# Kernel tuning notes

Hardware: AMD Instinct MI355X
Metric: run time of the kernel (lower is better)

Reference implementation:

```python
import jax, jax.numpy as jnp
import numpy as np

N_NODES = 100000
N_EDGES = 1200000
N_GRAPHS = 500
IN_DIM, HID, OUT = 128, 64, 16


def setup_inputs() -> dict:
    key = jax.random.key(0)
    ks = jax.random.split(key, 10)
    x = jax.random.normal(ks[0], (N_NODES, IN_DIM), dtype=jnp.float32)
    edge_index = jax.random.randint(ks[1], (2, N_EDGES), 0, N_NODES, dtype=jnp.int64)
    batch = jnp.sort(jax.random.randint(ks[2], (N_NODES,), 0, N_GRAPHS, dtype=jnp.int64))
    # Glorot-style init for GCN linear weights, zero bias (PyG default)
    def glorot(k, fan_in, fan_out):
        s = jnp.sqrt(6.0 / (fan_in + fan_out))
        return jax.random.uniform(k, (fan_in, fan_out), jnp.float32, -s, s)
    W1 = glorot(ks[3], IN_DIM, HID); b1 = jnp.zeros((HID,), jnp.float32)
    W2 = glorot(ks[4], HID, HID);    b2 = jnp.zeros((HID,), jnp.float32)
    W3 = glorot(ks[5], HID, OUT);    b3 = jnp.zeros((OUT,), jnp.float32)
    return {"x": x, "edge_index": edge_index, "batch": batch,
            "W1": W1, "b1": b1, "W2": W2, "b2": b2, "W3": W3, "b3": b3}


def gcn_conv(x, src, dst, deg_inv_sqrt, W, b, n_nodes):
    # PyG GCNConv: h = x @ W; aggregate with sym-normalized A+I; add bias.
    h = x @ W  # [N, F_out]
    norm = deg_inv_sqrt[src] * deg_inv_sqrt[dst]            # [E]
    msg = h[src] * norm[:, None]                            # gather + scale
    agg = jax.ops.segment_sum(msg, dst, num_segments=n_nodes)
    agg = agg + h * (deg_inv_sqrt * deg_inv_sqrt)[:, None]  # self-loop term
    return agg + b


def reference(x, edge_index, batch, W1, b1, W2, b2, W3, b3):
    n = x.shape[0]
    src, dst = edge_index[0], edge_index[1]
    # degree of A + I (count incoming edges at dst, plus self-loop)
    deg = 1.0 + jax.ops.segment_sum(jnp.ones_like(src, dtype=x.dtype), dst, num_segments=n)
    dis = deg ** -0.5  # deg >= 1 so always finite
    h = gcn_conv(x, src, dst, dis, W1, b1, n)
    h = jax.nn.relu(h)
    h = gcn_conv(h, src, dst, dis, W2, b2, n)
    h = jax.nn.relu(h)
    h = gcn_conv(h, src, dst, dis, W3, b3, n)
    # global_mean_pool over graph ids
    sums = jax.ops.segment_sum(h, batch, num_segments=N_GRAPHS)
    counts = jax.ops.segment_sum(jnp.ones((n,), h.dtype), batch, num_segments=N_GRAPHS)
    return sums / jnp.clip(counts, 1.0)[:, None]
```

## Files before the change

### kernel.cpp

```cpp
#include <hip/hip_runtime.h>
#include <hip/hip_bf16.h>
#include <hip/hip_fp16.h>

#define IN_DIM 128
#define HID    64
#define OUTF   16
#define NGRAPH 500

#define CE    2048
#define NRNG  8
#define CAP   512
#define NG    32
#define RSZ   12544

__device__ __forceinline__ uint2 f4_to_h4(float4 a) {
    __half2 lo = __floats2half2_rn(a.x, a.y);
    __half2 hi = __floats2half2_rn(a.z, a.w);
    uint2 r;
    r.x = *(unsigned*)&lo;
    r.y = *(unsigned*)&hi;
    return r;
}
__device__ __forceinline__ float4 h4_to_f4(uint2 q) {
    __half2 a = *(__half2*)&q.x, b = *(__half2*)&q.y;
    float2 fa = __half22float2(a), fb = __half22float2(b);
    return make_float4(fa.x, fa.y, fb.x, fb.y);
}
__device__ __forceinline__ void h8_to_f8(uint4 p, float4& f0, float4& f1) {
    __half2 a = *(__half2*)&p.x, b = *(__half2*)&p.y;
    __half2 c = *(__half2*)&p.z, d = *(__half2*)&p.w;
    float2 fa = __half22float2(a), fb = __half22float2(b);
    float2 fc = __half22float2(c), fd = __half22float2(d);
    f0 = make_float4(fa.x, fa.y, fb.x, fb.y);
    f1 = make_float4(fc.x, fc.y, fd.x, fd.y);
}

template<int K>
__global__ __launch_bounds__(256, 4) void gemm64_kernel(const float* __restrict__ X,
                                                        const float* __restrict__ W,
                                                        __half* __restrict__ Hh, int N) {
    constexpr int BK = 64;
    constexpr int PAD = 4;
    constexpr int LDX = BK + PAD;
    constexpr int K4 = K / 4;
    __shared__ float sX[64 * LDX];
    __shared__ float sW[BK * 64];
    const int tid = threadIdx.x;
    const int row0 = blockIdx.x * 64;
    const int tc = tid & 15;
    const int tr = tid >> 4;

    const float4* W4 = (const float4*)W;
    const float4* X4 = (const float4*)X;
    float4* sW4 = (float4*)sW;

    float4 acc0 = {0,0,0,0}, acc1 = {0,0,0,0}, acc2 = {0,0,0,0}, acc3 = {0,0,0,0};

    for (int k0 = 0; k0 < K; k0 += BK) {
        for (int i = tid; i < BK * 16; i += 256) sW4[i] = W4[k0 * 16 + i];
        for (int i = tid; i < 64 * (BK / 4); i += 256) {
            int r = i >> 4, kk = i & 15;
            int gr = row0 + r;
            float4 v = {0.f, 0.f, 0.f, 0.f};
            if (gr < N) v = X4[(long long)gr * K4 + (k0 >> 2) + kk];
            *(float4*)&sX[r * LDX + kk * 4] = v;
        }
        __syncthreads();

        const float* sX0 = &sX[(tr * 4) * LDX];
#pragma unroll 4
        for (int k = 0; k < BK; k += 4) {
            float4 x0 = *(const float4*)&sX0[k];
            float4 x1 = *(const float4*)&sX0[LDX + k];
            float4 x2 = *(const float4*)&sX0[2 * LDX + k];
            float4 x3 = *(const float4*)&sX0[3 * LDX + k];
            float4 w0 = sW4[(k + 0) * 16 + tc];
            float4 w1 = sW4[(k + 1) * 16 + tc];
            float4 w2 = sW4[(k + 2) * 16 + tc];
            float4 w3 = sW4[(k + 3) * 16 + tc];
            acc0.x += x0.x * w0.x; acc0.y += x0.x * w0.y; acc0.z += x0.x * w0.z; acc0.w += x0.x * w0.w;
            acc1.x += x1.x * w0.x; acc1.y += x1.x * w0.y; acc1.z += x1.x * w0.z; acc1.w += x1.x * w0.w;
            acc2.x += x2.x * w0.x; acc2.y += x2.x * w0.y; acc2.z += x2.x * w0.z; acc2.w += x2.x * w0.w;
            acc3.x += x3.x * w0.x; acc3.y += x3.x * w0.y; acc3.z += x3.x * w0.z; acc3.w += x3.x * w0.w;
            acc0.x += x0.y * w1.x; acc0.y += x0.y * w1.y; acc0.z += x0.y * w1.z; acc0.w += x0.y * w1.w;
            acc1.x += x1.y * w1.x; acc1.y += x1.y * w1.y; acc1.z += x1.y * w1.z; acc1.w += x1.y * w1.w;
            acc2.x += x2.y * w1.x; acc2.y += x2.y * w1.y; acc2.z += x2.y * w1.z; acc2.w += x2.y * w1.w;
            acc3.x += x3.y * w1.x; acc3.y += x3.y * w1.y; acc3.z += x3.y * w1.z; acc3.w += x3.y * w1.w;
            acc0.x += x0.z * w2.x; acc0.y += x0.z * w2.y; acc0.z += x0.z * w2.z; acc0.w += x0.z * w2.w;
            acc1.x += x1.z * w2.x; acc1.y += x1.z * w2.y; acc1.z += x1.z * w2.z; acc1.w += x1.z * w2.w;
            acc2.x += x2.z * w2.x; acc2.y += x2.z * w2.y; acc2.z += x2.z * w2.z; acc2.w += x2.z * w2.w;
            acc3.x += x3.z * w2.x; acc3.y += x3.z * w2.y; acc3.z += x3.z * w2.z; acc3.w += x3.z * w2.w;
            acc0.x += x0.w * w3.x; acc0.y += x0.w * w3.y; acc0.z += x0.w * w3.z; acc0.w += x0.w * w3.w;
            acc1.x += x1.w * w3.x; acc1.y += x1.w * w3.y; acc1.z += x1.w * w3.z; acc1.w += x1.w * w3.w;
            acc2.x += x2.w * w3.x; acc2.y += x2.w * w3.y; acc2.z += x2.w * w3.z; acc2.w += x2.w * w3.w;
            acc3.x += x3.w * w3.x; acc3.y += x3.w * w3.y; acc3.z += x3.w * w3.z; acc3.w += x3.w * w3.w;
        }
        __syncthreads();
    }

    uint2* Hh2 = (uint2*)Hh;
    int r0 = row0 + tr * 4;
    if (r0 + 0 < N) Hh2[(long long)(r0 + 0) * 16 + tc] = f4_to_h4(acc0);
    if (r0 + 1 < N) Hh2[(long long)(r0 + 1) * 16 + tc] = f4_to_h4(acc1);
    if (r0 + 2 < N) Hh2[(long long)(r0 + 2) * 16 + tc] = f4_to_h4(acc2);
    if (r0 + 3 < N) Hh2[(long long)(r0 + 3) * 16 + tc] = f4_to_h4(acc3);
}

template<int K, int F>
__global__ __launch_bounds__(256) void gemm_kernel(const float* __restrict__ X,
                                                   const float* __restrict__ W,
                                                   __half* __restrict__ Hh, int N) {
    constexpr int C4 = F / 4;
    constexpr int ROWS = 256 / C4;
    constexpr int K4 = K / 4;
    constexpr int LDX4 = K4 + 1;
    __shared__ float4 sW[K * C4];
    __shared__ float4 sX4[ROWS * LDX4];
    const int tid = threadIdx.x;
    const float4* W4 = (const float4*)W;
    for (int i = tid; i < K * C4; i += 256) sW[i] = W4[i];
    const int row0 = blockIdx.x * ROWS;
    const float4* X4 = (const float4*)X;
    for (int i = tid; i < ROWS * K4; i += 256) {
        int r = i / K4, kk = i - r * K4;
        int gr = row0 + r;
        float4 z = {0.f, 0.f, 0.f, 0.f};
        sX4[r * LDX4 + kk] = (gr < N) ? X4[(long long)gr * K4 + kk] : z;
    }
    __syncthreads();
    const int r = tid / C4, c4 = tid - (tid / C4) * C4;
    const float* sXr = (const float*)&sX4[r * LDX4];
    float4 acc = {0.f, 0.f, 0.f, 0.f};
#pragma unroll
    for (int k = 0; k < K; ++k) {
        float xv = sXr[k];
        float4 wv = sW[k * C4 + c4];
        acc.x += xv * wv.x; acc.y += xv * wv.y;
        acc.z += xv * wv.z; acc.w += xv * wv.w;
    }
    const int gr = row0 + r;
    if (gr < N) ((uint2*)Hh)[(long long)gr * C4 + c4] = f4_to_h4(acc);
}

__global__ __launch_bounds__(256) void part_kernel(const int* __restrict__ src,
                                                   const int* __restrict__ dst,
                                                   uint2* __restrict__ seg,
                                                   int* __restrict__ segcnt,
                                                   int E, int rangeSize) {
    __shared__ uint2 sSeg[NRNG][CAP];
    __shared__ int sCnt[NRNG];
    const int tid = threadIdx.x;
    if (tid < NRNG) sCnt[tid] = 0;
    __syncthreads();
    const int base = blockIdx.x * CE + tid;
    int d[8], s[8];
#pragma unroll
    for (int k = 0; k < 8; ++k) {
        int e = base + k * 256;
        d[k] = (e < E) ? dst[e] : -1;
        s[k] = (e < E) ? src[e] : 0;
    }
#pragma unroll
    for (int k = 0; k < 8; ++k) {
        if (d[k] >= 0) {
            int r = d[k] / rangeSize;
            int li = atomicAdd(&sCnt[r], 1);
            if (li < CAP) sSeg[r][li] = make_uint2((unsigned)s[k], (unsigned)d[k]);
        }
    }
    __syncthreads();
    for (int r = 0; r < NRNG; ++r) {
        int n = sCnt[r] < CAP ? sCnt[r] : CAP;
        uint2* out = seg + ((size_t)(blockIdx.x * NRNG + r)) * CAP;
        for (int i = tid; i < n; i += 256) out[i] = sSeg[r][i];
        if (tid == 0) segcnt[blockIdx.x * NRNG + r] = n;
    }
}

__global__ __launch_bounds__(256) void count_kernel(const uint2* __restrict__ seg,
                                                    const int* __restrict__ segcnt,
                                                    int* __restrict__ cnt,
                                                    int N, int rangeSize, int nchunks) {
    __shared__ int hist[RSZ];
    const int r = blockIdx.x & (NRNG - 1);
    const int g = blockIdx.x >> 3;
    const int cpg = (nchunks + NG - 1) / NG;
    const int c0 = g * cpg;
    const int c1 = (c0 + cpg < nchunks) ? c0 + cpg : nchunks;
    for (int i = threadIdx.x; i < rangeSize; i += 256) hist[i] = 0;
    __syncthreads();
    const int base = r * rangeSize;
    for (int c = c0; c < c1; ++c) {
        const int si = c * NRNG + r;
        const int n = segcnt[si];
        const uint2* s = seg + (size_t)si * CAP;
        for (int i = threadIdx.x; i < n; i += 256)
            atomicAdd(&hist[(int)s[i].y - base], 1);
    }
    __syncthreads();
    const int lim = (base + rangeSize <= N) ? rangeSize : (N - base);
    for (int i = threadIdx.x; i < lim; i += 256)
        cnt[(size_t)g * N + base + i] = hist[i];
}

__global__ __launch_bounds__(256) void nodescan_kernel(int* __restrict__ cnt,
                                                       int* __restrict__ degi, int N) {
    const int q = blockIdx.x * 256 + threadIdx.x;
    const int n0 = q * 4;
    if (n0 >= N) return;
    if ((N & 3) == 0 && n0 + 3 < N) {
        int4* c4 = (int4*)cnt;
        const int N4 = N >> 2;
        int4 run = {0, 0, 0, 0};
#pragma unroll
        for (int g = 0; g < NG; ++g) {
            const size_t idx = (size_t)g * N4 + q;
            int4 c = c4[idx];
            c4[idx] = run;
            run.x += c.x; run.y += c.y; run.z += c.z; run.w += c.w;
        }
        ((int4*)degi)[q] = run;
    } else {
        const int nend = (n0 + 4 < N) ? n0 + 4 : N;
        for (int n = n0; n < nend; ++n) {
            int run = 0;
            for (int g = 0; g < NG; ++g) {
                const size_t idx = (size_t)g * N + n;
                int c = cnt[idx];
                cnt[idx] = run;
                run += c;
            }
            degi[n] = run;
        }
    }
}

__global__ __launch_bounds__(1024) void scan1_kernel(const int* __restrict__ degi,
                                                     int* __restrict__ rowptr,
                                                     int* __restrict__ aux,
                                                     float* __restrict__ dis,
                                                     float* __restrict__ pool0, int N) {
    if (blockIdx.x == 0) {
        for (int i = threadIdx.x; i < NGRAPH * OUTF + NGRAPH; i += 1024) pool0[i] = 0.f;
    }
    __shared__ int s[1024];
    int i = blockIdx.x * 1024 + threadIdx.x;
    int v = (i < N) ? degi[i] : 0;
    if (i < N) dis[i] = rsqrtf(1.0f + (float)v);
    s[threadIdx.x] = v;
    __syncthreads();
    for (int off = 1; off < 1024; off <<= 1) {
        int t = (threadIdx.x >= off) ? s[threadIdx.x - off] : 0;
        __syncthreads();
        s[threadIdx.x] += t;
        __syncthreads();
    }
    if (i < N) rowptr[i] = s[threadIdx.x] - v;
    if (threadIdx.x == 1023) aux[blockIdx.x] = s[1023];
}

__global__ __launch_bounds__(1024) void scan3_kernel(int* __restrict__ rowptr,
                                                     const int* __restrict__ aux,
                                                     int N, int nb) {
    __shared__ int s[128];
    const int t = threadIdx.x;
    if (t < 128) s[t] = (t < nb) ? aux[t] : 0;
    __syncthreads();
    for (int off = 1; off < 128; off <<= 1) {
        int v = (t >= off && t < 128) ? s[t - off] : 0;
        __syncthreads();
        if (t < 128) s[t] += v;
        __syncthreads();
    }
    int add = (blockIdx.x == 0) ? 0 : s[blockIdx.x - 1];
    int i = blockIdx.x * 1024 + t;
    if (i < N) rowptr[i] += add;
}

__global__ __launch_bounds__(256) void scatter_kernel(const uint2* __restrict__ seg,
                                                      const int* __restrict__ segcnt,
                                                      const int* __restrict__ cntp,
                                                      const int* __restrict__ rowptr,
                                                      int* __restrict__ csr_src,
                                                      int N, int rangeSize, int nchunks) {
    __shared__ int hist[RSZ];
    const int r = blockIdx.x & (NRNG - 1);
    const int g = blockIdx.x >> 3;
    const int cpg = (nchunks + NG - 1) / NG;
    const int c0 = g * cpg;
    const int c1 = (c0 + cpg < nchunks) ? c0 + cpg : nchunks;
    for (int i = threadIdx.x; i < rangeSize; i += 256) hist[i] = 0;
    __syncthreads();
    const int base = r * rangeSize;
    for (int c = c0; c < c1; ++c) {
        const int si = c * NRNG + r;
        const int n = segcnt[si];
        const uint2* s = seg + (size_t)si * CAP;
        for (int i = threadIdx.x; i < n; i += 256) {
            uint2 v = s[i];
            const int d = (int)v.y;
            const int rank = atomicAdd(&hist[d - base], 1);
            csr_src[rowptr[d] + cntp[(size_t)g * N + d] + rank] = (int)v.x;
        }
    }
}

template<bool RELU>
__global__ __launch_bounds__(256) void agg64_kernel(const __half* __restrict__ Hh,
                                                    const int* __restrict__ rowptr,
                                                    const int* __restrict__ csr_src,
                                                    const float* __restrict__ dis,
                                                    const float4* __restrict__ b4,
                                                    float4* __restrict__ out4, int N, int E) {
    const int tid = threadIdx.x;
    const int lane = tid & 63;
    const int node = blockIdx.x * 16 + (tid >> 6) * 4 + (lane >> 4);
    const int g2 = (lane >> 3) & 1;
    const int c = lane & 7;
    if (node >= N) return;
    const uint4* Hh4 = (const uint4*)Hh;
    float dd = dis[node];
    int i0 = rowptr[node];
    int i1 = (node + 1 < N) ? rowptr[node + 1] : E;
    float4 a0 = {0.f, 0.f, 0.f, 0.f}, a1 = {0.f, 0.f, 0.f, 0.f};
    int i = i0 + g2;
    int iB = i + 2;
    int sA = (i < i1) ? csr_src[i] : 0;
    int sB = (iB < i1) ? csr_src[iB] : 0;
    uint4 pA = make_uint4(0u, 0u, 0u, 0u);
    float wA = 0.f;
    if (i < i1) {
        pA = Hh4[(long long)sA * 8 + c];
        wA = dis[sA] * dd;
    }
    while (i < i1) {
        const int iC = i + 4;
        int sC = (iC < i1) ? csr_src[iC] : 0;
        uint4 pB = Hh4[(long long)sB * 8 + c];
        float wB = (iB < i1) ? dis[sB] * dd : 0.f;
        float4 v0, v1;
        h8_to_f8(pA, v0, v1);
        a0.x += v0.x * wA; a0.y += v0.y * wA; a0.z += v0.z * wA; a0.w += v0.w * wA;
        a1.x += v1.x * wA; a1.y += v1.y * wA; a1.z += v1.z * wA; a1.w += v1.w * wA;
        i = iB; iB = iC; sA = sB; sB = sC; pA = pB; wA = wB;
    }
    a0.x += __shfl_xor(a0.x, 8); a0.y += __shfl_xor(a0.y, 8);
    a0.z += __shfl_xor(a0.z, 8); a0.w += __shfl_xor(a0.w, 8);
    a1.x += __shfl_xor(a1.x, 8); a1.y += __shfl_xor(a1.y, 8);
    a1.z += __shfl_xor(a1.z, 8); a1.w += __shfl_xor(a1.w, 8);
    if (g2 == 0) {
        float sl = dd * dd;
        uint4 ps = Hh4[(long long)node * 8 + c];
        float4 h0, h1;
        h8_to_f8(ps, h0, h1);
        float4 bb0 = b4[2 * c], bb1 = b4[2 * c + 1];
        a0.x += h0.x * sl + bb0.x; a0.y += h0.y * sl + bb0.y;
        a0.z += h0.z * sl + bb0.z; a0.w += h0.w * sl + bb0.w;
        a1.x += h1.x * sl + bb1.x; a1.y += h1.y * sl + bb1.y;
        a1.z += h1.z * sl + bb1.z; a1.w += h1.w * sl + bb1.w;
        if (RELU) {
            a0.x = fmaxf(a0.x, 0.f); a0.y = fmaxf(a0.y, 0.f);
            a0.z = fmaxf(a0.z, 0.f); a0.w = fmaxf(a0.w, 0.f);
            a1.x = fmaxf(a1.x, 0.f); a1.y = fmaxf(a1.y, 0.f);
            a1.z = fmaxf(a1.z, 0.f); a1.w = fmaxf(a1.w, 0.f);
        }
        out4[(long long)node * 16 + 2 * c] = a0;
        out4[(long long)node * 16 + 2 * c + 1] = a1;
    }
}

template<bool RELU>
__global__ __launch_bounds__(256) void agg16_kernel(const __half* __restrict__ Hh,
                                                    const int* __restrict__ rowptr,
                                                    const int* __restrict__ csr_src,
                                                    const float* __restrict__ dis,
                                                    const float4* __restrict__ b4,
                                                    float4* __restrict__ out4, int N, int E) {
    const int tid = threadIdx.x;
    const int lane = tid & 63;
    const int node = blockIdx.x * 32 + (tid >> 6) * 8 + (lane >> 3);
    const int g2 = (lane >> 2) & 1;
    const int c = lane & 3;
    if (node >= N) return;
    const uint2* Hh2 = (const uint2*)Hh;
    float dd = dis[node];
    int i0 = rowptr[node];
    int i1 = (node + 1 < N) ? rowptr[node + 1] : E;
    float4 acc = {0.f, 0.f, 0.f, 0.f};
    int i = i0 + g2;
    int iB = i + 2;
    int sA = (i < i1) ? csr_src[i] : 0;
    int sB = (iB < i1) ? csr_src[iB] : 0;
    uint2 pA = make_uint2(0u, 0u);
    float wA = 0.f;
    if (i < i1) {
        pA = Hh2[(long long)sA * 4 + c];
        wA = dis[sA] * dd;
    }
    while (i < i1) {
        const int iC = i + 4;
        int sC = (iC < i1) ? csr_src[iC] : 0;
        uint2 pB = Hh2[(long long)sB * 4 + c];
        float wB = (iB < i1) ? dis[sB] * dd : 0.f;
        float4 v = h4_to_f4(pA);
        acc.x += v.x * wA; acc.y += v.y * wA;
        acc.z += v.z * wA; acc.w += v.w * wA;
        i = iB; iB = iC; sA = sB; sB = sC; pA = pB; wA = wB;
    }
    acc.x += __shfl_xor(acc.x, 4);
    acc.y += __shfl_xor(acc.y, 4);
    acc.z += __shfl_xor(acc.z, 4);
    acc.w += __shfl_xor(acc.w, 4);
    if (g2 == 0) {
        float4 h = h4_to_f4(Hh2[(long long)node * 4 + c]);
        float sl = dd * dd;
        float4 bb = b4[c];
        acc.x += h.x * sl + bb.x; acc.y += h.y * sl + bb.y;
        acc.z += h.z * sl + bb.z; acc.w += h.w * sl + bb.w;
        if (RELU) {
            acc.x = fmaxf(acc.x, 0.f); acc.y = fmaxf(acc.y, 0.f);
            acc.z = fmaxf(acc.z, 0.f); acc.w = fmaxf(acc.w, 0.f);
        }
        out4[(long long)node * 4 + c] = acc;
    }
}

__global__ __launch_bounds__(256) void pool_kernel(const float4* __restrict__ H4,
                                                   const int* __restrict__ batch,
                                                   float* __restrict__ sums,
                                                   float* __restrict__ cnts, int N) {
    __shared__ float sBin[16][16];
    __shared__ float sCnt[16];
    const int t = threadIdx.x;
    sBin[t >> 4][t & 15] = 0.f;
    if (t < 16) sCnt[t] = 0.f;
    __syncthreads();
    const int n0 = blockIdx.x * 256;
    const int g0 = batch[n0];
    const int nl = t >> 2;
    const int f4 = t & 3;
    float4 acc = {0.f, 0.f, 0.f, 0.f};
    float cnt = 0.f;
    int curli = -1;
    for (int j = 0; j < 4; ++j) {
        int node = n0 + nl * 4 + j;
        if (node >= N) break;
        int li = batch[node] - g0;
        if (li != curli) {
            if (curli >= 0) {
                if (curli < 16) {
                    float* bp = &sBin[curli][f4 * 4];
                    atomicAdd(bp + 0, acc.x); atomicAdd(bp + 1, acc.y);
                    atomicAdd(bp + 2, acc.z); atomicAdd(bp + 3, acc.w);
                    if (f4 == 0) atomicAdd(&sCnt[curli], cnt);
                } else {
                    float* gp = &sums[(g0 + curli) * OUTF + f4 * 4];
                    atomicAdd(gp + 0, acc.x); atomicAdd(gp + 1, acc.y);
                    atomicAdd(gp + 2, acc.z); atomicAdd(gp + 3, acc.w);
                    if (f4 == 0) atomicAdd(&cnts[g0 + curli], cnt);
                }
            }
            acc.x = acc.y = acc.z = acc.w = 0.f; cnt = 0.f; curli = li;
        }
        float4 v = H4[(long long)node * 4 + f4];
        acc.x += v.x; acc.y += v.y; acc.z += v.z; acc.w += v.w;
        cnt += 1.f;
    }
    if (curli >= 0) {
        if (curli < 16) {
            float* bp = &sBin[curli][f4 * 4];
            atomicAdd(bp + 0, acc.x); atomicAdd(bp + 1, acc.y);
            atomicAdd(bp + 2, acc.z); atomicAdd(bp + 3, acc.w);
            if (f4 == 0) atomicAdd(&sCnt[curli], cnt);
        } else {
            float* gp = &sums[(g0 + curli) * OUTF + f4 * 4];
            atomicAdd(gp + 0, acc.x); atomicAdd(gp + 1, acc.y);
            atomicAdd(gp + 2, acc.z); atomicAdd(gp + 3, acc.w);
            if (f4 == 0) atomicAdd(&cnts[g0 + curli], cnt);
        }
    }
    __syncthreads();
    int bg = t >> 4, bf = t & 15;
    int g = g0 + bg;
    if (g < NGRAPH) {
        float v = sBin[bg][bf];
        if (v != 0.f) atomicAdd(&sums[g * OUTF + bf], v);
        if (bf == 0) {
            float c = sCnt[bg];
            if (c != 0.f) atomicAdd(&cnts[g], c);
        }
    }
}

__global__ void divide_kernel(const float* __restrict__ sums, const float* __restrict__ counts,
                              float* __restrict__ out) {
    int i = blockIdx.x * blockDim.x + threadIdx.x;
    if (i < NGRAPH * OUTF) out[i] = sums[i] / fmaxf(counts[i >> 4], 1.0f);
}

extern "C" void kernel_launch(void* const* d_in, const int* in_sizes, int n_in,
                              void* d_out, int out_size, void* d_ws, size_t ws_size,
                              hipStream_t stream) {
    const float* x     = (const float*)d_in[0];
    const int*   ei    = (const int*)d_in[1];
    const int*   batch = (const int*)d_in[2];
    const float* W1 = (const float*)d_in[3];
    const float* b1 = (const float*)d_in[4];
    const float* W2 = (const float*)d_in[5];
    const float* b2 = (const float*)d_in[6];
    const float* W3 = (const float*)d_in[7];
    const float* b3 = (const float*)d_in[8];
    float* out = (float*)d_out;

    const int N = in_sizes[2];
    const int E = in_sizes[1] / 2;
    const int* src = ei;
    const int* dst = ei + E;

    const int nchunks = (E + CE - 1) / CE;
    const int NGB = NG * NRNG;

    float*    ws      = (float*)d_ws;
    float*    dis     = ws;
    float*    bufA    = dis + N;
    float*    bufB    = bufA + (size_t)N * HID;
    float*    sums    = bufB + (size_t)N * HID;
    float*    cnts    = sums + NGRAPH * OUTF;
    int*      degi    = (int*)(cnts + NGRAPH);
    int*      rowptr  = degi + N;
    int*      csr_src = rowptr + N;
    int*      segcnt  = csr_src + E;
    int*      aux     = segcnt + nchunks * NRNG;
    uint2*    seg     = (uint2*)bufB;
    int*      cntmat  = (int*)bufA;
    __half*   Hh      = (__half*)bufA;

    const int B = 256;
    const int nb = (N + 1023) / 1024;
    const int rangeSize = (N + NRNG - 1) / NRNG;

    part_kernel<<<nchunks, B, 0, stream>>>(src, dst, seg, segcnt, E, rangeSize);
    count_kernel<<<NGB, B, 0, stream>>>(seg, segcnt, cntmat, N, rangeSize, nchunks);
    nodescan_kernel<<<((N + 3) / 4 + 255) / 256, B, 0, stream>>>(cntmat, degi, N);
    scan1_kernel<<<nb, 1024, 0, stream>>>(degi, rowptr, aux, dis, sums, N);
    scan3_kernel<<<nb, 1024, 0, stream>>>(rowptr, aux, N, nb);
    scatter_kernel<<<NGB, B, 0, stream>>>(seg, segcnt, cntmat, rowptr, csr_src, N, rangeSize, nchunks);

    gemm64_kernel<IN_DIM><<<(N + 63) / 64, B, 0, stream>>>(x, W1, Hh, N);
    agg64_kernel<true><<<(N + 15) / 16, B, 0, stream>>>(Hh, rowptr, csr_src,
                                                        dis, (const float4*)b1, (float4*)bufB, N, E);

    gemm64_kernel<HID><<<(N + 63) / 64, B, 0, stream>>>(bufB, W2, Hh, N);
    agg64_kernel<true><<<(N + 15) / 16, B, 0, stream>>>(Hh, rowptr, csr_src,
                                                        dis, (const float4*)b2, (float4*)bufB, N, E);

    gemm_kernel<HID, OUTF><<<(N + 63) / 64, B, 0, stream>>>(bufB, W3, Hh, N);
    agg16_kernel<false><<<(N + 31) / 32, B, 0, stream>>>(Hh, rowptr, csr_src,
                                                         dis, (const float4*)b3, (float4*)bufB, N, E);

    pool_kernel<<<(N + 255) / 256, B, 0, stream>>>((const float4*)bufB, batch, sums, cnts, N);
    divide_kernel<<<(NGRAPH * OUTF + B - 1) / B, B, 0, stream>>>(sums, cnts, out);
}
```

Baseline: 302.9 us.

## Fuse GCN aggregation with next-layer GEMM and final aggregation with pooling

New measurement: 309.9 us. +2.3%, slower.

```diff
diff --git a/kernel.cpp b/kernel.cpp
--- a/kernel.cpp
+++ b/kernel.cpp
@@ -33,6 +33,34 @@
     float2 fc = __half22float2(c), fd = __half22float2(d);
     f0 = make_float4(fa.x, fa.y, fb.x, fb.y);
     f1 = make_float4(fc.x, fc.y, fd.x, fd.y);
+}
+
+__device__ __forceinline__ void agg64_edges(const uint4* __restrict__ Hh4,
+                                            const int* __restrict__ csr_src,
+                                            const float* __restrict__ dis,
+                                            int i0, int i1, int g2, int c, float dd,
+                                            float4& a0, float4& a1) {
+    int i = i0 + g2;
+    int iB = i + 2;
+    int sA = (i < i1) ? csr_src[i] : 0;
+    int sB = (iB < i1) ? csr_src[iB] : 0;
+    uint4 pA = make_uint4(0u, 0u, 0u, 0u);
+    float wA = 0.f;
+    if (i < i1) {
+        pA = Hh4[(long long)sA * 8 + c];
+        wA = dis[sA] * dd;
+    }
+    while (i < i1) {
+        const int iC = i + 4;
+        int sC = (iC < i1) ? csr_src[iC] : 0;
+        uint4 pB = Hh4[(long long)sB * 8 + c];
+        float wB = (iB < i1) ? dis[sB] * dd : 0.f;
+        float4 v0, v1;
+        h8_to_f8(pA, v0, v1);
+        a0.x += v0.x * wA; a0.y += v0.y * wA; a0.z += v0.z * wA; a0.w += v0.w * wA;
+        a1.x += v1.x * wA; a1.y += v1.y * wA; a1.z += v1.z * wA; a1.w += v1.w * wA;
+        i = iB; iB = iC; sA = sB; sB = sC; pA = pB; wA = wB;
+    }
 }
 
 template<int K>
@@ -106,40 +134,163 @@
     if (r0 + 3 < N) Hh2[(long long)(r0 + 3) * 16 + tc] = f4_to_h4(acc3);
 }
 
-template<int K, int F>
-__global__ __launch_bounds__(256) void gemm_kernel(const float* __restrict__ X,
-                                                   const float* __restrict__ W,
-                                                   __half* __restrict__ Hh, int N) {
-    constexpr int C4 = F / 4;
-    constexpr int ROWS = 256 / C4;
-    constexpr int K4 = K / 4;
-    constexpr int LDX4 = K4 + 1;
-    __shared__ float4 sW[K * C4];
-    __shared__ float4 sX4[ROWS * LDX4];
+__global__ __launch_bounds__(256, 4) void agg_gemm64_kernel(
+        const __half* __restrict__ Hin, const int* __restrict__ rowptr,
+        const int* __restrict__ csr_src, const float* __restrict__ dis,
+        const float4* __restrict__ b4, const float* __restrict__ W,
+        __half* __restrict__ Hout, int N, int E) {
+    constexpr int LDX = 68;
+    __shared__ float sX[64 * LDX];
+    __shared__ float sW[64 * 64];
     const int tid = threadIdx.x;
-    const float4* W4 = (const float4*)W;
-    for (int i = tid; i < K * C4; i += 256) sW[i] = W4[i];
-    const int row0 = blockIdx.x * ROWS;
-    const float4* X4 = (const float4*)X;
-    for (int i = tid; i < ROWS * K4; i += 256) {
-        int r = i / K4, kk = i - r * K4;
-        int gr = row0 + r;
-        float4 z = {0.f, 0.f, 0.f, 0.f};
-        sX4[r * LDX4 + kk] = (gr < N) ? X4[(long long)gr * K4 + kk] : z;
-    }
-    __syncthreads();
-    const int r = tid / C4, c4 = tid - (tid / C4) * C4;
-    const float* sXr = (const float*)&sX4[r * LDX4];
+    const int row0 = blockIdx.x * 64;
+    {
+        const float4* W4 = (const float4*)W;
+        float4* sW4 = (float4*)sW;
+        for (int i = tid; i < 1024; i += 256) sW4[i] = W4[i];
+    }
+    const int lane = tid & 63;
+    const int widx = tid >> 6;
+    const int g2 = (lane >> 3) & 1;
+    const int c = lane & 7;
+    const uint4* Hh4 = (const uint4*)Hin;
+    for (int b = 0; b < 4; ++b) {
+        const int nl = b * 16 + widx * 4 + (lane >> 4);
+        const int node = row0 + nl;
+        if (node < N) {
+            float dd = dis[node];
+            int i0 = rowptr[node];
+            int i1 = (node + 1 < N) ? rowptr[node + 1] : E;
+            float4 a0 = {0,0,0,0}, a1 = {0,0,0,0};
+            agg64_edges(Hh4, csr_src, dis, i0, i1, g2, c, dd, a0, a1);
+            a0.x += __shfl_xor(a0.x, 8); a0.y += __shfl_xor(a0.y, 8);
+            a0.z += __shfl_xor(a0.z, 8); a0.w += __shfl_xor(a0.w, 8);
+            a1.x += __shfl_xor(a1.x, 8); a1.y += __shfl_xor(a1.y, 8);
+            a1.z += __shfl_xor(a1.z, 8); a1.w += __shfl_xor(a1.w, 8);
+            if (g2 == 0) {
+                float sl = dd * dd;
+                uint4 ps = Hh4[(long long)node * 8 + c];
+                float4 h0, h1;
+                h8_to_f8(ps, h0, h1);
+                float4 bb0 = b4[2 * c], bb1 = b4[2 * c + 1];
+                a0.x += h0.x * sl + bb0.x; a0.y += h0.y * sl + bb0.y;
+                a0.z += h0.z * sl + bb0.z; a0.w += h0.w * sl + bb0.w;
+                a1.x += h1.x * sl + bb1.x; a1.y += h1.y * sl + bb1.y;
+                a1.z += h1.z * sl + bb1.z; a1.w += h1.w * sl + bb1.w;
+                a0.x = fmaxf(a0.x, 0.f); a0.y = fmaxf(a0.y, 0.f);
+                a0.z = fmaxf(a0.z, 0.f); a0.w = fmaxf(a0.w, 0.f);
+                a1.x = fmaxf(a1.x, 0.f); a1.y = fmaxf(a1.y, 0.f);
+                a1.z = fmaxf(a1.z, 0.f); a1.w = fmaxf(a1.w, 0.f);
+                *(float4*)&sX[nl * LDX + 8 * c] = a0;
+                *(float4*)&sX[nl * LDX + 8 * c + 4] = a1;
+            }
+        }
+    }
+    __syncthreads();
+    const int tc = tid & 15;
+    const int tr = tid >> 4;
+    const float* sX0 = &sX[(tr * 4) * LDX];
+    const float4* sW4 = (const float4*)sW;
+    float4 acc0 = {0,0,0,0}, acc1 = {0,0,0,0}, acc2 = {0,0,0,0}, acc3 = {0,0,0,0};
+#pragma unroll 4
+    for (int k = 0; k < 64; k += 4) {
+        float4 x0 = *(const float4*)&sX0[k];
+        float4 x1 = *(const float4*)&sX0[LDX + k];
+        float4 x2 = *(const float4*)&sX0[2 * LDX + k];
+        float4 x3 = *(const float4*)&sX0[3 * LDX + k];
+        float4 w0 = sW4[(k + 0) * 16 + tc];
+        float4 w1 = sW4[(k + 1) * 16 + tc];
+        float4 w2 = sW4[(k + 2) * 16 + tc];
+        float4 w3 = sW4[(k + 3) * 16 + tc];
+        acc0.x += x0.x * w0.x; acc0.y += x0.x * w0.y; acc0.z += x0.x * w0.z; acc0.w += x0.x * w0.w;
+        acc1.x += x1.x * w0.x; acc1.y += x1.x * w0.y; acc1.z += x1.x * w0.z; acc1.w += x1.x * w0.w;
+        acc2.x += x2.x * w0.x; acc2.y += x2.x * w0.y; acc2.z += x2.x * w0.z; acc2.w += x2.x * w0.w;
+        acc3.x += x3.x * w0.x; acc3.y += x3.x * w0.y; acc3.z += x3.x * w0.z; acc3.w += x3.x * w0.w;
+        acc0.x += x0.y * w1.x; acc0.y += x0.y * w1.y; acc0.z += x0.y * w1.z; acc0.w += x0.y * w1.w;
+        acc1.x += x1.y * w1.x; acc1.y += x1.y * w1.y; acc1.z += x1.y * w1.z; acc1.w += x1.y * w1.w;
+        acc2.x += x2.y * w1.x; acc2.y += x2.y * w1.y; acc2.z += x2.y * w1.z; acc2.w += x2.y * w1.w;
+        acc3.x += x3.y * w1.x; acc3.y += x3.y * w1.y; acc3.z += x3.y * w1.z; acc3.w += x3.y * w1.w;
+        acc0.x += x0.z * w2.x; acc0.y += x0.z * w2.y; acc0.z += x0.z * w2.z; acc0.w += x0.z * w2.w;
+        acc1.x += x1.z * w2.x; acc1.y += x1.z * w2.y; acc1.z += x1.z * w2.z; acc1.w += x1.z * w2.w;
+        acc2.x += x2.z * w2.x; acc2.y += x2.z * w2.y; acc2.z += x2.z * w2.z; acc2.w += x2.z * w2.w;
+        acc3.x += x3.z * w2.x; acc3.y += x3.z * w2.y; acc3.z += x3.z * w2.z; acc3.w += x3.z * w2.w;
+        acc0.x += x0.w * w3.x; acc0.y += x0.w * w3.y; acc0.z += x0.w * w3.z; acc0.w += x0.w * w3.w;
+        acc1.x += x1.w * w3.x; acc1.y += x1.w * w3.y; acc1.z += x1.w * w3.z; acc1.w += x1.w * w3.w;
+        acc2.x += x2.w * w3.x; acc2.y += x2.w * w3.y; acc2.z += x2.w * w3.z; acc2.w += x2.w * w3.w;
+        acc3.x += x3.w * w3.x; acc3.y += x3.w * w3.y; acc3.z += x3.w * w3.z; acc3.w += x3.w * w3.w;
+    }
+    uint2* Ho = (uint2*)Hout;
+    int r0 = row0 + tr * 4;
+    if (r0 + 0 < N) Ho[(long long)(r0 + 0) * 16 + tc] = f4_to_h4(acc0);
+    if (r0 + 1 < N) Ho[(long long)(r0 + 1) * 16 + tc] = f4_to_h4(acc1);
+    if (r0 + 2 < N) Ho[(long long)(r0 + 2) * 16 + tc] = f4_to_h4(acc2);
+    if (r0 + 3 < N) Ho[(long long)(r0 + 3) * 16 + tc] = f4_to_h4(acc3);
+}
+
+__global__ __launch_bounds__(256) void agg_gemm16_kernel(
+        const __half* __restrict__ Hin, const int* __restrict__ rowptr,
+        const int* __restrict__ csr_src, const float* __restrict__ dis,
+        const float4* __restrict__ b4, const float* __restrict__ W,
+        __half* __restrict__ Hout, int N, int E) {
+    constexpr int LDX = 68;
+    __shared__ float sX[64 * LDX];
+    __shared__ float4 sW3[64 * 4];
+    const int tid = threadIdx.x;
+    const int row0 = blockIdx.x * 64;
+    {
+        const float4* W4 = (const float4*)W;
+        if (tid < 256) sW3[tid] = W4[tid];
+    }
+    const int lane = tid & 63;
+    const int widx = tid >> 6;
+    const int g2 = (lane >> 3) & 1;
+    const int c = lane & 7;
+    const uint4* Hh4 = (const uint4*)Hin;
+    for (int b = 0; b < 4; ++b) {
+        const int nl = b * 16 + widx * 4 + (lane >> 4);
+        const int node = row0 + nl;
+        if (node < N) {
+            float dd = dis[node];
+            int i0 = rowptr[node];
+            int i1 = (node + 1 < N) ? rowptr[node + 1] : E;
+            float4 a0 = {0,0,0,0}, a1 = {0,0,0,0};
+            agg64_edges(Hh4, csr_src, dis, i0, i1, g2, c, dd, a0, a1);
+            a0.x += __shfl_xor(a0.x, 8); a0.y += __shfl_xor(a0.y, 8);
+            a0.z += __shfl_xor(a0.z, 8); a0.w += __shfl_xor(a0.w, 8);
+            a1.x += __shfl_xor(a1.x, 8); a1.y += __shfl_xor(a1.y, 8);
+            a1.z += __shfl_xor(a1.z, 8); a1.w += __shfl_xor(a1.w, 8);
+            if (g2 == 0) {
+                float sl = dd * dd;
+                uint4 ps = Hh4[(long long)node * 8 + c];
+                float4 h0, h1;
+                h8_to_f8(ps, h0, h1);
+                float4 bb0 = b4[2 * c], bb1 = b4[2 * c + 1];
+                a0.x += h0.x * sl + bb0.x; a0.y += h0.y * sl + bb0.y;
+                a0.z += h0.z * sl + bb0.z; a0.w += h0.w * sl + bb0.w;
+                a1.x += h1.x * sl + bb1.x; a1.y += h1.y * sl + bb1.y;
+                a1.z += h1.z * sl + bb1.z; a1.w += h1.w * sl + bb1.w;
+                a0.x = fmaxf(a0.x, 0.f); a0.y = fmaxf(a0.y, 0.f);
+                a0.z = fmaxf(a0.z, 0.f); a0.w = fmaxf(a0.w, 0.f);
+                a1.x = fmaxf(a1.x, 0.f); a1.y = fmaxf(a1.y, 0.f);
+                a1.z = fmaxf(a1.z, 0.f); a1.w = fmaxf(a1.w, 0.f);
+                *(float4*)&sX[nl * LDX + 8 * c] = a0;
+                *(float4*)&sX[nl * LDX + 8 * c + 4] = a1;
+            }
+        }
+    }
+    __syncthreads();
+    const int r = tid >> 2, c4 = tid & 3;
+    const float* sXr = &sX[r * LDX];
     float4 acc = {0.f, 0.f, 0.f, 0.f};
 #pragma unroll
-    for (int k = 0; k < K; ++k) {
+    for (int k = 0; k < 64; ++k) {
         float xv = sXr[k];
-        float4 wv = sW[k * C4 + c4];
+        float4 wv = sW3[k * 4 + c4];
         acc.x += xv * wv.x; acc.y += xv * wv.y;
         acc.z += xv * wv.z; acc.w += xv * wv.w;
     }
     const int gr = row0 + r;
-    if (gr < N) ((uint2*)Hh)[(long long)gr * C4 + c4] = f4_to_h4(acc);
+    if (gr < N) ((uint2*)Hout)[(long long)gr * 4 + c4] = f4_to_h4(acc);
 }
 
 __global__ __launch_bounds__(256) void part_kernel(const int* __restrict__ src,
@@ -305,140 +456,71 @@
     }
 }
 
-template<bool RELU>
-__global__ __launch_bounds__(256) void agg64_kernel(const __half* __restrict__ Hh,
-                                                    const int* __restrict__ rowptr,
-                                                    const int* __restrict__ csr_src,
-                                                    const float* __restrict__ dis,
-                                                    const float4* __restrict__ b4,
-                                                    float4* __restrict__ out4, int N, int E) {
+__global__ __launch_bounds__(256) void agg_pool_kernel(const __half* __restrict__ Hin,
+                                                       const int* __restrict__ rowptr,
+                                                       const int* __restrict__ csr_src,
+                                                       const float* __restrict__ dis,
+                                                       const float4* __restrict__ b4,
+                                                       const int* __restrict__ batch,
+                                                       float* __restrict__ sums,
+                                                       float* __restrict__ cnts, int N, int E) {
+    __shared__ float sH[256 * 16];
+    __shared__ float sBin[16][16];
+    __shared__ float sCnt[16];
     const int tid = threadIdx.x;
+    const int n0 = blockIdx.x * 256;
+    sBin[tid >> 4][tid & 15] = 0.f;
+    if (tid < 16) sCnt[tid] = 0.f;
     const int lane = tid & 63;
-    const int node = blockIdx.x * 16 + (tid >> 6) * 4 + (lane >> 4);
-    const int g2 = (lane >> 3) & 1;
-    const int c = lane & 7;
-    if (node >= N) return;
-    const uint4* Hh4 = (const uint4*)Hh;
-    float dd = dis[node];
-    int i0 = rowptr[node];
-    int i1 = (node + 1 < N) ? rowptr[node + 1] : E;
-    float4 a0 = {0.f, 0.f, 0.f, 0.f}, a1 = {0.f, 0.f, 0.f, 0.f};
-    int i = i0 + g2;
-    int iB = i + 2;
-    int sA = (i < i1) ? csr_src[i] : 0;
-    int sB = (iB < i1) ? csr_src[iB] : 0;
-    uint4 pA = make_uint4(0u, 0u, 0u, 0u);
-    float wA = 0.f;
-    if (i < i1) {
-        pA = Hh4[(long long)sA * 8 + c];
-        wA = dis[sA] * dd;
-    }
-    while (i < i1) {
-        const int iC = i + 4;
-        int sC = (iC < i1) ? csr_src[iC] : 0;
-        uint4 pB = Hh4[(long long)sB * 8 + c];
-        float wB = (iB < i1) ? dis[sB] * dd : 0.f;
-        float4 v0, v1;
-        h8_to_f8(pA, v0, v1);
-        a0.x += v0.x * wA; a0.y += v0.y * wA; a0.z += v0.z * wA; a0.w += v0.w * wA;
-        a1.x += v1.x * wA; a1.y += v1.y * wA; a1.z += v1.z * wA; a1.w += v1.w * wA;
-        i = iB; iB = iC; sA = sB; sB = sC; pA = pB; wA = wB;
-    }
-    a0.x += __shfl_xor(a0.x, 8); a0.y += __shfl_xor(a0.y, 8);
-    a0.z += __shfl_xor(a0.z, 8); a0.w += __shfl_xor(a0.w, 8);
-    a1.x += __shfl_xor(a1.x, 8); a1.y += __shfl_xor(a1.y, 8);
-    a1.z += __shfl_xor(a1.z, 8); a1.w += __shfl_xor(a1.w, 8);
-    if (g2 == 0) {
-        float sl = dd * dd;
-        uint4 ps = Hh4[(long long)node * 8 + c];
-        float4 h0, h1;
-        h8_to_f8(ps, h0, h1);
-        float4 bb0 = b4[2 * c], bb1 = b4[2 * c + 1];
-        a0.x += h0.x * sl + bb0.x; a0.y += h0.y * sl + bb0.y;
-        a0.z += h0.z * sl + bb0.z; a0.w += h0.w * sl + bb0.w;
-        a1.x += h1.x * sl + bb1.x; a1.y += h1.y * sl + bb1.y;
-        a1.z += h1.z * sl + bb1.z; a1.w += h1.w * sl + bb1.w;
-        if (RELU) {
-            a0.x = fmaxf(a0.x, 0.f); a0.y = fmaxf(a0.y, 0.f);
-            a0.z = fmaxf(a0.z, 0.f); a0.w = fmaxf(a0.w, 0.f);
-            a1.x = fmaxf(a1.x, 0.f); a1.y = fmaxf(a1.y, 0.f);
-            a1.z = fmaxf(a1.z, 0.f); a1.w = fmaxf(a1.w, 0.f);
-        }
-        out4[(long long)node * 16 + 2 * c] = a0;
-        out4[(long long)node * 16 + 2 * c + 1] = a1;
-    }
-}
-
-template<bool RELU>
-__global__ __launch_bounds__(256) void agg16_kernel(const __half* __restrict__ Hh,
-                                                    const int* __restrict__ rowptr,
-                                                    const int* __restrict__ csr_src,
-                                                    const float* __restrict__ dis,
-                                                    const float4* __restrict__ b4,
-                                                    float4* __restrict__ out4, int N, int E) {
-    const int tid = threadIdx.x;
-    const int lane = tid & 63;
-    const int node = blockIdx.x * 32 + (tid >> 6) * 8 + (lane >> 3);
+    const int widx = tid >> 6;
     const int g2 = (lane >> 2) & 1;
     const int c = lane & 3;
-    if (node >= N) return;
-    const uint2* Hh2 = (const uint2*)Hh;
-    float dd = dis[node];
-    int i0 = rowptr[node];
-    int i1 = (node + 1 < N) ? rowptr[node + 1] : E;
-    float4 acc = {0.f, 0.f, 0.f, 0.f};
-    int i = i0 + g2;
-    int iB = i + 2;
-    int sA = (i < i1) ? csr_src[i] : 0;
-    int sB = (iB < i1) ? csr_src[iB] : 0;
-    uint2 pA = make_uint2(0u, 0u);
-    float wA = 0.f;
-    if (i < i1) {
-        pA = Hh2[(long long)sA * 4 + c];
-        wA = dis[sA] * dd;
-    }
-    while (i < i1) {
-        const int iC = i + 4;
-        int sC = (iC < i1) ? csr_src[iC] : 0;
-        uint2 pB = Hh2[(long long)sB * 4 + c];
-        float wB = (iB < i1) ? dis[sB] * dd : 0.f;
-        float4 v = h4_to_f4(pA);
-        acc.x += v.x * wA; acc.y += v.y * wA;
-        acc.z += v.z * wA; acc.w += v.w * wA;
-        i = iB; iB = iC; sA = sB; sB = sC; pA = pB; wA = wB;
-    }
-    acc.x += __shfl_xor(acc.x, 4);
-    acc.y += __shfl_xor(acc.y, 4);
-    acc.z += __shfl_xor(acc.z, 4);
-    acc.w += __shfl_xor(acc.w, 4);
-    if (g2 == 0) {
-        float4 h = h4_to_f4(Hh2[(long long)node * 4 + c]);
-        float sl = dd * dd;
-        float4 bb = b4[c];
-        acc.x += h.x * sl + bb.x; acc.y += h.y * sl + bb.y;
-        acc.z += h.z * sl + bb.z; acc.w += h.w * sl + bb.w;
-        if (RELU) {
-            acc.x = fmaxf(acc.x, 0.f); acc.y = fmaxf(acc.y, 0.f);
-            acc.z = fmaxf(acc.z, 0.f); acc.w = fmaxf(acc.w, 0.f);
-        }
-        out4[(long long)node * 4 + c] = acc;
-    }
-}
-
-__global__ __launch_bounds__(256) void pool_kernel(const float4* __restrict__ H4,
-                                                   const int* __restrict__ batch,
-                                                   float* __restrict__ sums,
-                                                   float* __restrict__ cnts, int N) {
-    __shared__ float sBin[16][16];
-    __shared__ float sCnt[16];
-    const int t = threadIdx.x;
-    sBin[t >> 4][t & 15] = 0.f;
-    if (t < 16) sCnt[t] = 0.f;
-    __syncthreads();
-    const int n0 = blockIdx.x * 256;
+    const uint2* Hh2 = (const uint2*)Hin;
+    for (int p = 0; p < 8; ++p) {
+        const int node = n0 + p * 32 + widx * 8 + (lane >> 3);
+        if (node < N) {
+            float dd = dis[node];
+            int i0 = rowptr[node];
+            int i1 = (node + 1 < N) ? rowptr[node + 1] : E;
+            float4 acc = {0.f, 0.f, 0.f, 0.f};
+            int i = i0 + g2;
+            int iB = i + 2;
+            int sA = (i < i1) ? csr_src[i] : 0;
+            int sB = (iB < i1) ? csr_src[iB] : 0;
+            uint2 pA = make_uint2(0u, 0u);
+            float wA = 0.f;
+            if (i < i1) {
+                pA = Hh2[(long long)sA * 4 + c];
+                wA = dis[sA] * dd;
+            }
+            while (i < i1) {
+                const int iC = i + 4;
+                int sC = (iC < i1) ? csr_src[iC] : 0;
+                uint2 pB = Hh2[(long long)sB * 4 + c];
+                float wB = (iB < i1) ? dis[sB] * dd : 0.f;
+                float4 v = h4_to_f4(pA);
+                acc.x += v.x * wA; acc.y += v.y * wA;
+                acc.z += v.z * wA; acc.w += v.w * wA;
+                i = iB; iB = iC; sA = sB; sB = sC; pA = pB; wA = wB;
+            }
+            acc.x += __shfl_xor(acc.x, 4);
+            acc.y += __shfl_xor(acc.y, 4);
+            acc.z += __shfl_xor(acc.z, 4);
+            acc.w += __shfl_xor(acc.w, 4);
+            if (g2 == 0) {
+                float4 h = h4_to_f4(Hh2[(long long)node * 4 + c]);
+                float sl = dd * dd;
+                float4 bb = b4[c];
+                acc.x += h.x * sl + bb.x; acc.y += h.y * sl + bb.y;
+                acc.z += h.z * sl + bb.z; acc.w += h.w * sl + bb.w;
+                *(float4*)&sH[(node - n0) * 16 + 4 * c] = acc;
+            }
+        }
+    }
+    __syncthreads();
     const int g0 = batch[n0];
-    const int nl = t >> 2;
-    const int f4 = t & 3;
+    const int nl = tid >> 2;
+    const int f4 = tid & 3;
     float4 acc = {0.f, 0.f, 0.f, 0.f};
     float cnt = 0.f;
     int curli = -1;
@@ -462,7 +544,7 @@
             }
             acc.x = acc.y = acc.z = acc.w = 0.f; cnt = 0.f; curli = li;
         }
-        float4 v = H4[(long long)node * 4 + f4];
+        float4 v = *(const float4*)&sH[(nl * 4 + j) * 16 + f4 * 4];
         acc.x += v.x; acc.y += v.y; acc.z += v.z; acc.w += v.w;
         cnt += 1.f;
     }
@@ -480,14 +562,14 @@
         }
     }
     __syncthreads();
-    int bg = t >> 4, bf = t & 15;
+    int bg = tid >> 4, bf = tid & 15;
     int g = g0 + bg;
     if (g < NGRAPH) {
         float v = sBin[bg][bf];
         if (v != 0.f) atomicAdd(&sums[g * OUTF + bf], v);
         if (bf == 0) {
-            float c = sCnt[bg];
-            if (c != 0.f) atomicAdd(&cnts[g], c);
+            float c2 = sCnt[bg];
+            if (c2 != 0.f) atomicAdd(&cnts[g], c2);
         }
     }
 }
@@ -533,7 +615,9 @@
     int*      aux     = segcnt + nchunks * NRNG;
     uint2*    seg     = (uint2*)bufB;
     int*      cntmat  = (int*)bufA;
-    __half*   Hh      = (__half*)bufA;
+    __half*   Hh1     = (__half*)bufA;
+    __half*   Hh2     = (__half*)bufB;
+    __half*   Hh3     = (__half*)bufA;
 
     const int B = 256;
     const int nb = (N + 1023) / 1024;
@@ -546,18 +630,15 @@
     scan3_kernel<<<nb, 1024, 0, stream>>>(rowptr, aux, N, nb);
     scatter_kernel<<<NGB, B, 0, stream>>>(seg, segcnt, cntmat, rowptr, csr_src, N, rangeSize, nchunks);
 
-    gemm64_kernel<IN_DIM><<<(N + 63) / 64, B, 0, stream>>>(x, W1, Hh, N);
-    agg64_kernel<true><<<(N + 15) / 16, B, 0, stream>>>(Hh, rowptr, csr_src,
-                                                        dis, (const float4*)b1, (float4*)bufB, N, E);
-
-    gemm64_kernel<HID><<<(N + 63) / 64, B, 0, stream>>>(bufB, W2, Hh, N);
-    agg64_kernel<true><<<(N + 15) / 16, B, 0, stream>>>(Hh, rowptr, csr_src,
-                                                        dis, (const float4*)b2, (float4*)bufB, N, E);
-
-    gemm_kernel<HID, OUTF><<<(N + 63) / 64, B, 0, stream>>>(bufB, W3, Hh, N);
-    agg16_kernel<false><<<(N + 31) / 32, B, 0, stream>>>(Hh, rowptr, csr_src,
-                                                         dis, (const float4*)b3, (float4*)bufB, N, E);
-
-    pool_kernel<<<(N + 255) / 256, B, 0, stream>>>((const float4*)bufB, batch, sums, cnts, N);
+    gemm64_kernel<IN_DIM><<<(N + 63) / 64, B, 0, stream>>>(x, W1, Hh1, N);
+
+    agg_gemm64_kernel<<<(N + 63) / 64, B, 0, stream>>>(Hh1, rowptr, csr_src, dis,
+                                                       (const float4*)b1, W2, Hh2, N, E);
+
+    agg_gemm16_kernel<<<(N + 63) / 64, B, 0, stream>>>(Hh2, rowptr, csr_src, dis,
+                                                       (const float4*)b2, W3, Hh3, N, E);
+
+    agg_pool_kernel<<<(N + 255) / 256, B, 0, stream>>>(Hh3, rowptr, csr_src, dis,
+                                                       (const float4*)b3, batch, sums, cnts, N, E);
     divide_kernel<<<(NGRAPH * OUTF + B - 1) / B, B, 0, stream>>>(sums, cnts, out);
 }
```

## Fuse per-node group scan into scan1 and double destination ranges

Applied to the files above, without the earlier changes.

Result: faster. 289.5 us (-4.4%).

```diff
diff --git a/kernel.cpp b/kernel.cpp
--- a/kernel.cpp
+++ b/kernel.cpp
@@ -8,10 +8,10 @@
 #define NGRAPH 500
 
 #define CE    2048
-#define NRNG  8
-#define CAP   512
+#define NRNG  16
+#define CAP   256
 #define NG    32
-#define RSZ   12544
+#define RSZ   6272
 
 __device__ __forceinline__ uint2 f4_to_h4(float4 a) {
     __half2 lo = __floats2half2_rn(a.x, a.y);
@@ -183,7 +183,7 @@
                                                     int N, int rangeSize, int nchunks) {
     __shared__ int hist[RSZ];
     const int r = blockIdx.x & (NRNG - 1);
-    const int g = blockIdx.x >> 3;
+    const int g = blockIdx.x / NRNG;
     const int cpg = (nchunks + NG - 1) / NG;
     const int c0 = g * cpg;
     const int c1 = (c0 + cpg < nchunks) ? c0 + cpg : nchunks;
@@ -203,39 +203,7 @@
         cnt[(size_t)g * N + base + i] = hist[i];
 }
 
-__global__ __launch_bounds__(256) void nodescan_kernel(int* __restrict__ cnt,
-                                                       int* __restrict__ degi, int N) {
-    const int q = blockIdx.x * 256 + threadIdx.x;
-    const int n0 = q * 4;
-    if (n0 >= N) return;
-    if ((N & 3) == 0 && n0 + 3 < N) {
-        int4* c4 = (int4*)cnt;
-        const int N4 = N >> 2;
-        int4 run = {0, 0, 0, 0};
-#pragma unroll
-        for (int g = 0; g < NG; ++g) {
-            const size_t idx = (size_t)g * N4 + q;
-            int4 c = c4[idx];
-            c4[idx] = run;
-            run.x += c.x; run.y += c.y; run.z += c.z; run.w += c.w;
-        }
-        ((int4*)degi)[q] = run;
-    } else {
-        const int nend = (n0 + 4 < N) ? n0 + 4 : N;
-        for (int n = n0; n < nend; ++n) {
-            int run = 0;
-            for (int g = 0; g < NG; ++g) {
-                const size_t idx = (size_t)g * N + n;
-                int c = cnt[idx];
-                cnt[idx] = run;
-                run += c;
-            }
-            degi[n] = run;
-        }
-    }
-}
-
-__global__ __launch_bounds__(1024) void scan1_kernel(const int* __restrict__ degi,
+__global__ __launch_bounds__(1024) void scan1_kernel(int* __restrict__ cnt,
                                                      int* __restrict__ rowptr,
                                                      int* __restrict__ aux,
                                                      float* __restrict__ dis,
@@ -245,8 +213,19 @@
     }
     __shared__ int s[1024];
     int i = blockIdx.x * 1024 + threadIdx.x;
-    int v = (i < N) ? degi[i] : 0;
-    if (i < N) dis[i] = rsqrtf(1.0f + (float)v);
+    int v = 0;
+    if (i < N) {
+        int run = 0;
+#pragma unroll
+        for (int g = 0; g < NG; ++g) {
+            const size_t idx = (size_t)g * N + i;
+            int c = cnt[idx];
+            cnt[idx] = run;
+            run += c;
+        }
+        v = run;
+        dis[i] = rsqrtf(1.0f + (float)v);
+    }
     s[threadIdx.x] = v;
     __syncthreads();
     for (int off = 1; off < 1024; off <<= 1) {
@@ -285,7 +264,7 @@
                                                       int N, int rangeSize, int nchunks) {
     __shared__ int hist[RSZ];
     const int r = blockIdx.x & (NRNG - 1);
-    const int g = blockIdx.x >> 3;
+    const int g = blockIdx.x / NRNG;
     const int cpg = (nchunks + NG - 1) / NG;
     const int c0 = g * cpg;
     const int c1 = (c0 + cpg < nchunks) ? c0 + cpg : nchunks;
@@ -526,8 +505,7 @@
     float*    bufB    = bufA + (size_t)N * HID;
     float*    sums    = bufB + (size_t)N * HID;
     float*    cnts    = sums + NGRAPH * OUTF;
-    int*      degi    = (int*)(cnts + NGRAPH);
-    int*      rowptr  = degi + N;
+    int*      rowptr  = (int*)(cnts + NGRAPH);
     int*      csr_src = rowptr + N;
     int*      segcnt  = csr_src + E;
     int*      aux     = segcnt + nchunks * NRNG;
@@ -541,8 +519,7 @@
 
     part_kernel<<<nchunks, B, 0, stream>>>(src, dst, seg, segcnt, E, rangeSize);
     count_kernel<<<NGB, B, 0, stream>>>(seg, segcnt, cntmat, N, rangeSize, nchunks);
-    nodescan_kernel<<<((N + 3) / 4 + 255) / 256, B, 0, stream>>>(cntmat, degi, N);
-    scan1_kernel<<<nb, 1024, 0, stream>>>(degi, rowptr, aux, dis, sums, N);
+    scan1_kernel<<<nb, 1024, 0, stream>>>(cntmat, rowptr, aux, dis, sums, N);
     scan3_kernel<<<nb, 1024, 0, stream>>>(rowptr, aux, N, nb);
     scatter_kernel<<<NGB, B, 0, stream>>>(seg, segcnt, cntmat, rowptr, csr_src, N, rangeSize, nchunks);
 
```
